# Optimization experiments

Hardware: AMD Instinct MI355X
Metric: run time of the kernel (lower is better)

## Reference

```python
import jax, jax.numpy as jnp
import numpy as np

HEADS = 8
DIM_HEAD = 64
QUERY_DIM = 512
INNER = HEADS * DIM_HEAD
DIAG_OFFSET = 1
T_TEMP = 1.0
NEG_INF = -1e9  # used via -inf below; kept for clarity


def setup_inputs() -> dict:
    key = jax.random.key(0)
    ks = jax.random.split(key, 8)
    b, s, f = 2, 2048, 16
    x = jax.random.normal(ks[0], (b, s, f, QUERY_DIM), dtype=jnp.float32)
    pos_bias = jax.random.normal(ks[1], (HEADS, f, f), dtype=jnp.float32)
    w_scale = 0.02
    Wq = jax.random.normal(ks[2], (QUERY_DIM, INNER), dtype=jnp.float32) * w_scale
    Wk = jax.random.normal(ks[3], (QUERY_DIM, INNER), dtype=jnp.float32) * w_scale
    Wv = jax.random.normal(ks[4], (QUERY_DIM, INNER), dtype=jnp.float32) * w_scale
    Wo = jax.random.normal(ks[5], (INNER, QUERY_DIM), dtype=jnp.float32) * w_scale
    bo = jax.random.normal(ks[6], (QUERY_DIM,), dtype=jnp.float32) * w_scale
    return {"x": x, "pos_bias": pos_bias, "Wq": Wq, "Wk": Wk, "Wv": Wv, "Wo": Wo, "bo": bo}


def reference(x, pos_bias, Wq, Wk, Wv, Wo, bo):
    # x: [b, s, f, c] -- temporal attention over the frame axis f per spatial token
    b, s, f, _ = x.shape
    scale = DIM_HEAD ** -0.5
    q = (x @ Wq).reshape(b, s, f, HEADS, DIM_HEAD)
    k = (x @ Wk).reshape(b, s, f, HEADS, DIM_HEAD)
    v = (x @ Wv).reshape(b, s, f, HEADS, DIM_HEAD)
    # scores over frames: [b, s, h, f_q, f_k]
    w = jnp.einsum('bsihd,bsjhd->bshij', q * scale, k)
    w = w + pos_bias[None, None]  # [h, f, f] relative position bias
    # attend_prev_only causal mask (strict, diag_offset=1)
    causal = jnp.triu(jnp.ones((f, f), dtype=jnp.float32), k=DIAG_OFFSET)
    w = w + jnp.where(causal == 1.0, -jnp.inf, 0.0)
    # faithful to source: subtract row max, then softmax with temperature
    w = w - jax.lax.stop_gradient(jnp.max(w, axis=-1, keepdims=True))
    p = jax.nn.softmax(w.astype(jnp.float32) / T_TEMP, axis=-1).astype(w.dtype)
    out = jnp.einsum('bshij,bsjhd->bsihd', p, v).reshape(b, s, f, INNER)
    return out @ Wo + bo
```

## Files before the change

### kernel.cpp

```cpp
#include <hip/hip_runtime.h>

typedef unsigned short u16;
typedef __attribute__((ext_vector_type(8))) unsigned short u16x8;
typedef __attribute__((ext_vector_type(8))) __bf16 bf16x8;
typedef __attribute__((ext_vector_type(4))) float f32x4;

#define M_ROWS 65536
#define KDIM   512
#define NKT    8

typedef __attribute__((address_space(1))) const void gconst_void;
typedef __attribute__((address_space(3))) void lds_void;

static __device__ __forceinline__ u16 f2bf(float f) {
  unsigned u = __builtin_bit_cast(unsigned, f);
  u += 0x7FFFu + ((u >> 16) & 1u);
  return (u16)(u >> 16);
}

static __device__ __forceinline__ f32x4 mfma_bf16(u16x8 a, u16x8 b, f32x4 c) {
  return __builtin_amdgcn_mfma_f32_16x16x32_bf16(
      __builtin_bit_cast(bf16x8, a), __builtin_bit_cast(bf16x8, b), c, 0, 0, 0);
}

__global__ void conv_x(const float* __restrict__ x, u16* __restrict__ xb) {
  const size_t t = (size_t)blockIdx.x * 256 + threadIdx.x;
  f32x4 a = *(const f32x4*)(x + t * 8);
  f32x4 b = *(const f32x4*)(x + t * 8 + 4);
  u16x8 w;
#pragma unroll
  for (int e = 0; e < 4; ++e) { w[e] = f2bf(a[e]); w[e + 4] = f2bf(b[e]); }
  *(u16x8*)(xb + t * 8) = w;
}

__global__ void convW_qkv_t(const float* __restrict__ Wq, const float* __restrict__ Wk,
                            const float* __restrict__ Wv, u16* __restrict__ Wt) {
  __shared__ float tile[32][33];
  const int bn = blockIdx.x * 32;
  const int bk = blockIdx.y * 32;
  const int tx = threadIdx.x & 31, ty = threadIdx.x >> 5;
  const float* W = (bn < 512) ? Wq : ((bn < 1024) ? Wk : Wv);
  const int coln = bn & 511;
#pragma unroll
  for (int r = 0; r < 32; r += 8)
    tile[ty + r][tx] = W[(size_t)(bk + ty + r) * 512 + coln + tx];
  __syncthreads();
#pragma unroll
  for (int r = 0; r < 32; r += 8)
    Wt[(size_t)(bn + ty + r) * 512 + bk + tx] = f2bf(tile[tx][ty + r]);
}

__global__ void convWo_t(const float* __restrict__ Wo, u16* __restrict__ Wt) {
  __shared__ float tile[32][33];
  const int bn = blockIdx.x * 32;
  const int bk = blockIdx.y * 32;
  const int tx = threadIdx.x & 31, ty = threadIdx.x >> 5;
#pragma unroll
  for (int r = 0; r < 32; r += 8)
    tile[ty + r][tx] = Wo[(size_t)(bk + ty + r) * 512 + bn + tx];
  __syncthreads();
#pragma unroll
  for (int r = 0; r < 32; r += 8)
    Wt[(size_t)(bn + ty + r) * 512 + bk + tx] = f2bf(tile[tx][ty + r]);
}

__global__ __launch_bounds__(512, 4)
void gemm_qkv_attn(const u16* __restrict__ A, const u16* __restrict__ Wt,
                   const float* __restrict__ pos_bias, u16* __restrict__ attnbuf) {
  __shared__ __attribute__((aligned(16))) u16 smem[40960];
  u16* Ab   = smem;
  u16* Bb   = smem + 16384;
  u16* qkvT = smem;
  u16* Pl   = smem + 25600;

  const int tid  = threadIdx.x;
  const int lane = tid & 63;
  const int wid  = tid >> 6;
  const int wm   = wid >> 2;
  const int wn   = wid & 3;
  const int lg   = lane >> 4;
  const int lc   = lane & 15;
  const int srow = lane >> 3;
  const int sg   = (lane & 7) ^ srow;

  const int nwg  = gridDim.x;
  const int cpx  = nwg >> 3;
  const int flat = blockIdx.x;
  const int swz  = (flat & 7) * cpx + (flat >> 3);
  const int mt   = swz >> 3;
  const int h    = swz & 7;
  const int row0 = mt * 128;

  auto stageA = [&](int buf, int unit, int kt) {
    const int rl = unit * 64 + wid * 8;
    const u16* src = A + (size_t)(row0 + rl + srow) * KDIM + kt * 64 + sg * 8;
    __builtin_amdgcn_global_load_lds((gconst_void*)src,
                                     (lds_void*)&Ab[buf * 8192 + rl * 64], 16, 0, 0);
  };
  auto stageB = [&](int buf, int unit, int kt) {
    const int rl = unit * 64 + wid * 8;
    const int grow = unit * 512 + h * 64 + wid * 8 + srow;
    const u16* src = Wt + (size_t)grow * KDIM + kt * 64 + sg * 8;
    __builtin_amdgcn_global_load_lds((gconst_void*)src,
                                     (lds_void*)&Bb[buf * 12288 + rl * 64], 16, 0, 0);
  };

  f32x4 acc[4][3];
#pragma unroll
  for (int mi = 0; mi < 4; ++mi)
#pragma unroll
    for (int ni = 0; ni < 3; ++ni) acc[mi][ni] = (f32x4){0.f, 0.f, 0.f, 0.f};

  stageA(0, 0, 0); stageA(0, 1, 0);
  stageB(0, 0, 0); stageB(0, 1, 0); stageB(0, 2, 0);
  asm volatile("s_waitcnt vmcnt(0)" ::: "memory");
  __builtin_amdgcn_s_barrier();

  for (int t = 0; t < NKT; ++t) {
    const int  c   = t & 1;
    const bool pre = (t + 1) < NKT;

    if (pre) {
      stageA(c ^ 1, 0, t + 1); stageA(c ^ 1, 1, t + 1);
      stageB(c ^ 1, 0, t + 1); stageB(c ^ 1, 1, t + 1); stageB(c ^ 1, 2, t + 1);
    }

#pragma unroll
    for (int ks = 0; ks < 2; ++ks) {
      const int gsw = ((ks * 4 + lg) ^ (lc & 7)) << 3;
      u16x8 bfr[3], af[4];
#pragma unroll
      for (int ni = 0; ni < 3; ++ni)
        bfr[ni] = *(const u16x8*)&Bb[c * 12288 + (wn * 48 + ni * 16 + lc) * 64 + gsw];
#pragma unroll
      for (int i = 0; i < 4; ++i)
        af[i] = *(const u16x8*)&Ab[c * 8192 + (wm * 64 + i * 16 + lc) * 64 + gsw];
#pragma unroll
      for (int i = 0; i < 4; ++i)
#pragma unroll
        for (int ni = 0; ni < 3; ++ni)
          acc[i][ni] = mfma_bf16(af[i], bfr[ni], acc[i][ni]);
    }

    asm volatile("s_waitcnt vmcnt(0)" ::: "memory");
    __builtin_amdgcn_s_barrier();
  }

#pragma unroll
  for (int mi = 0; mi < 4; ++mi)
#pragma unroll
    for (int ni = 0; ni < 3; ++ni) {
      const int col = wn * 48 + ni * 16 + lc;
      const int rb  = wm * 64 + mi * 16 + lg * 4;
#pragma unroll
      for (int r = 0; r < 4; ++r)
        qkvT[(rb + r) * 200 + col] = f2bf(acc[mi][ni][r]);
    }
  __syncthreads();

  const float scale = 0.125f;
  const f32x4 zf = {0.f, 0.f, 0.f, 0.f};
  const int rb = wid * 16;
  const int qb = (rb + lc) * 200;

  u16x8 aq0 = *(const u16x8*)&qkvT[qb + 0  + lg * 8];
  u16x8 aq1 = *(const u16x8*)&qkvT[qb + 32 + lg * 8];
  u16x8 bk0 = *(const u16x8*)&qkvT[qb + 64 + lg * 8];
  u16x8 bk1 = *(const u16x8*)&qkvT[qb + 96 + lg * 8];
  f32x4 s = mfma_bf16(aq0, bk0, zf);
  s = mfma_bf16(aq1, bk1, s);

  const int pb = wid * 256;
#pragma unroll
  for (int r = 0; r < 4; ++r) {
    const int i = lg * 4 + r;
    float sv = s[r] * scale + pos_bias[h * 256 + i * 16 + lc];
    if (lc > i) sv = -1e30f;
    float m = sv;
#pragma unroll
    for (int off = 8; off >= 1; off >>= 1) m = fmaxf(m, __shfl_xor(m, off));
    float e = __expf(sv - m);
    float sm = e;
#pragma unroll
    for (int off = 8; off >= 1; off >>= 1) sm += __shfl_xor(sm, off);
    Pl[pb + i * 16 + lc] = f2bf(e / sm);
  }
  asm volatile("s_waitcnt lgkmcnt(0)" ::: "memory");

  u16x8 ap = {0, 0, 0, 0, 0, 0, 0, 0};
  if (lane < 32) ap = *(const u16x8*)&Pl[pb + lc * 16 + lg * 8];

#pragma unroll
  for (int nd = 0; nd < 4; ++nd) {
    u16x8 bv = {0, 0, 0, 0, 0, 0, 0, 0};
    if (lane < 32) {
#pragma unroll
      for (int jj = 0; jj < 8; ++jj) {
        const int j = lg * 8 + jj;
        bv[jj] = qkvT[(rb + j) * 200 + 128 + nd * 16 + lc];
      }
    }
    f32x4 o = mfma_bf16(ap, bv, zf);
#pragma unroll
    for (int r = 0; r < 4; ++r) {
      const int i = lg * 4 + r;
      attnbuf[(size_t)(row0 + rb + i) * 512 + h * 64 + nd * 16 + lc] = f2bf(o[r]);
    }
  }
}

__global__ __launch_bounds__(512, 2)
void gemm_out(const u16* __restrict__ A, const u16* __restrict__ Bt,
              float* __restrict__ C, const float* __restrict__ bias) {
  __shared__ __attribute__((aligned(16))) u16 smem[65536];
  u16* Ab = smem;
  u16* Bb = smem + 49152;

  const int tid  = threadIdx.x;
  const int lane = tid & 63;
  const int wid  = tid >> 6;
  const int wm   = wid >> 1;
  const int wn   = wid & 1;
  const int lg   = lane >> 4;
  const int lc   = lane & 15;
  const int srow = lane >> 3;
  const int sg   = (lane & 7) ^ srow;

  const int nwg  = gridDim.x;
  const int cpx  = nwg >> 3;
  const int flat = blockIdx.x;
  const int swz  = (flat & 7) * cpx + (flat >> 3);
  const int mt   = swz >> 2;
  const int nt   = swz & 3;
  const int row0 = mt * 256, col0 = nt * 128;

  auto stageA = [&](int buf, int unit, int kt) {
    const int rl = unit * 64 + wid * 8;
    const u16* src = A + (size_t)(row0 + rl + srow) * KDIM + kt * 64 + sg * 8;
    __builtin_amdgcn_global_load_lds((gconst_void*)src,
                                     (lds_void*)&Ab[buf * 16384 + rl * 64], 16, 0, 0);
  };
  auto stageB = [&](int buf, int unit, int kt) {
    const int rl = unit * 64 + wid * 8;
    const u16* src = Bt + (size_t)(col0 + rl + srow) * KDIM + kt * 64 + sg * 8;
    __builtin_amdgcn_global_load_lds((gconst_void*)src,
                                     (lds_void*)&Bb[buf * 8192 + rl * 64], 16, 0, 0);
  };

  f32x4 acc[4][4];
#pragma unroll
  for (int mi = 0; mi < 4; ++mi)
#pragma unroll
    for (int ni = 0; ni < 4; ++ni) acc[mi][ni] = (f32x4){0.f, 0.f, 0.f, 0.f};

#pragma unroll
  for (int u = 0; u < 4; ++u) stageA(0, u, 0);
#pragma unroll
  for (int u = 0; u < 2; ++u) stageB(0, u, 0);
#pragma unroll
  for (int u = 0; u < 4; ++u) stageA(1, u, 1);

  for (int t = 0; t < NKT; ++t) {
    const int  ab   = t % 3;
    const int  bb   = t & 1;
    const bool preB = (t + 1) < NKT;
    const bool preA = (t + 2) < NKT;
    const int  ab2  = (t + 2) % 3;

    if (t < NKT - 1) asm volatile("s_waitcnt vmcnt(4)" ::: "memory");
    else             asm volatile("s_waitcnt vmcnt(0)" ::: "memory");
    __builtin_amdgcn_s_barrier();

    if (preB) { stageB(bb ^ 1, 0, t + 1); stageB(bb ^ 1, 1, t + 1); }
    if (preA) { stageA(ab2, 0, t + 2); stageA(ab2, 1, t + 2);
                stageA(ab2, 2, t + 2); stageA(ab2, 3, t + 2); }

#pragma unroll
    for (int ks = 0; ks < 2; ++ks) {
      const int gsw = ((ks * 4 + lg) ^ (lc & 7)) << 3;
      u16x8 bfr[4], af[4];
#pragma unroll
      for (int ni = 0; ni < 4; ++ni)
        bfr[ni] = *(const u16x8*)&Bb[bb * 8192 + (wn * 64 + ni * 16 + lc) * 64 + gsw];
#pragma unroll
      for (int i = 0; i < 4; ++i)
        af[i] = *(const u16x8*)&Ab[ab * 16384 + (wm * 64 + i * 16 + lc) * 64 + gsw];
#pragma unroll
      for (int i = 0; i < 4; ++i)
#pragma unroll
        for (int ni = 0; ni < 4; ++ni)
          acc[i][ni] = mfma_bf16(af[i], bfr[ni], acc[i][ni]);
    }
  }

  const int gmb = row0 + wm * 64;
  const int gnb = col0 + wn * 64;
#pragma unroll
  for (int mi = 0; mi < 4; ++mi)
#pragma unroll
    for (int ni = 0; ni < 4; ++ni) {
      const int gm = gmb + mi * 16 + lg * 4;
      const int gn = gnb + ni * 16 + lc;
      const float bv = bias[gn];
      f32x4 v = acc[mi][ni];
#pragma unroll
      for (int r = 0; r < 4; ++r) C[(size_t)(gm + r) * 512 + gn] = v[r] + bv;
    }
}

extern "C" void kernel_launch(void* const* d_in, const int* in_sizes, int n_in,
                              void* d_out, int out_size, void* d_ws, size_t ws_size,
                              hipStream_t stream) {
  const float* x        = (const float*)d_in[0];
  const float* pos_bias = (const float*)d_in[1];
  const float* Wq       = (const float*)d_in[2];
  const float* Wk       = (const float*)d_in[3];
  const float* Wv       = (const float*)d_in[4];
  const float* Wo       = (const float*)d_in[5];
  const float* bo       = (const float*)d_in[6];
  float* out            = (float*)d_out;

  u16* xb      = (u16*)d_ws;
  u16* attnbuf = xb + (size_t)M_ROWS * 512;
  u16* Wo_t    = attnbuf + (size_t)M_ROWS * 512;
  u16* Wqkv_t  = (u16*)d_out;

  conv_x<<<dim3(M_ROWS * KDIM / (256 * 8)), dim3(256), 0, stream>>>(x, xb);
  convW_qkv_t<<<dim3(48, 16), dim3(256), 0, stream>>>(Wq, Wk, Wv, Wqkv_t);
  gemm_qkv_attn<<<dim3(4096), dim3(512), 0, stream>>>(xb, Wqkv_t, pos_bias, attnbuf);
  convWo_t<<<dim3(16, 16), dim3(256), 0, stream>>>(Wo, Wo_t);
  gemm_out<<<dim3(1024), dim3(512), 0, stream>>>(attnbuf, Wo_t, out, bo);
}
```

Measured before the change: 210.7 us.

## Shrink output GEMM tile to 128x128 with double-buffered LDS and higher occupancy

The output projection GEMM moves from a 256x128 tile with a triple-buffered A and double-buffered B pipeline to a 128x128 tile with a simple double buffer. The grid doubles to 2048 workgroups, LDS per block drops from 128KB to 64KB, and launch bounds ask for 4 blocks per CU. The goal is more waves per CU to hide latency, and a grid that spreads more evenly over the CUs. In exchange, each block reuses the B tile across fewer rows, so global traffic per FLOP goes up. Each iteration also now ends with a full vmcnt(0) wait and barrier, which reduces how much loads overlap with compute.

```diff
diff --git a/kernel.cpp b/kernel.cpp
--- a/kernel.cpp
+++ b/kernel.cpp
@@ -209,18 +209,18 @@
   }
 }
 
-__global__ __launch_bounds__(512, 2)
+__global__ __launch_bounds__(512, 4)
 void gemm_out(const u16* __restrict__ A, const u16* __restrict__ Bt,
               float* __restrict__ C, const float* __restrict__ bias) {
-  __shared__ __attribute__((aligned(16))) u16 smem[65536];
+  __shared__ __attribute__((aligned(16))) u16 smem[32768];
   u16* Ab = smem;
-  u16* Bb = smem + 49152;
+  u16* Bb = smem + 16384;
 
   const int tid  = threadIdx.x;
   const int lane = tid & 63;
   const int wid  = tid >> 6;
-  const int wm   = wid >> 1;
-  const int wn   = wid & 1;
+  const int wm   = wid >> 2;
+  const int wn   = wid & 3;
   const int lg   = lane >> 4;
   const int lc   = lane & 15;
   const int srow = lane >> 3;
@@ -232,13 +232,13 @@
   const int swz  = (flat & 7) * cpx + (flat >> 3);
   const int mt   = swz >> 2;
   const int nt   = swz & 3;
-  const int row0 = mt * 256, col0 = nt * 128;
+  const int row0 = mt * 128, col0 = nt * 128;
 
   auto stageA = [&](int buf, int unit, int kt) {
     const int rl = unit * 64 + wid * 8;
     const u16* src = A + (size_t)(row0 + rl + srow) * KDIM + kt * 64 + sg * 8;
     __builtin_amdgcn_global_load_lds((gconst_void*)src,
-                                     (lds_void*)&Ab[buf * 16384 + rl * 64], 16, 0, 0);
+                                     (lds_void*)&Ab[buf * 8192 + rl * 64], 16, 0, 0);
   };
   auto stageB = [&](int buf, int unit, int kt) {
     const int rl = unit * 64 + wid * 8;
@@ -247,58 +247,53 @@
                                      (lds_void*)&Bb[buf * 8192 + rl * 64], 16, 0, 0);
   };
 
-  f32x4 acc[4][4];
+  f32x4 acc[4][2];
 #pragma unroll
   for (int mi = 0; mi < 4; ++mi)
 #pragma unroll
-    for (int ni = 0; ni < 4; ++ni) acc[mi][ni] = (f32x4){0.f, 0.f, 0.f, 0.f};
-
-#pragma unroll
-  for (int u = 0; u < 4; ++u) stageA(0, u, 0);
-#pragma unroll
-  for (int u = 0; u < 2; ++u) stageB(0, u, 0);
-#pragma unroll
-  for (int u = 0; u < 4; ++u) stageA(1, u, 1);
+    for (int ni = 0; ni < 2; ++ni) acc[mi][ni] = (f32x4){0.f, 0.f, 0.f, 0.f};
+
+  stageA(0, 0, 0); stageA(0, 1, 0);
+  stageB(0, 0, 0); stageB(0, 1, 0);
+  asm volatile("s_waitcnt vmcnt(0)" ::: "memory");
+  __builtin_amdgcn_s_barrier();
 
   for (int t = 0; t < NKT; ++t) {
-    const int  ab   = t % 3;
-    const int  bb   = t & 1;
-    const bool preB = (t + 1) < NKT;
-    const bool preA = (t + 2) < NKT;
-    const int  ab2  = (t + 2) % 3;
-
-    if (t < NKT - 1) asm volatile("s_waitcnt vmcnt(4)" ::: "memory");
-    else             asm volatile("s_waitcnt vmcnt(0)" ::: "memory");
-    __builtin_amdgcn_s_barrier();
-
-    if (preB) { stageB(bb ^ 1, 0, t + 1); stageB(bb ^ 1, 1, t + 1); }
-    if (preA) { stageA(ab2, 0, t + 2); stageA(ab2, 1, t + 2);
-                stageA(ab2, 2, t + 2); stageA(ab2, 3, t + 2); }
+    const int  c   = t & 1;
+    const bool pre = (t + 1) < NKT;
+
+    if (pre) {
+      stageA(c ^ 1, 0, t + 1); stageA(c ^ 1, 1, t + 1);
+      stageB(c ^ 1, 0, t + 1); stageB(c ^ 1, 1, t + 1);
+    }
 
 #pragma unroll
     for (int ks = 0; ks < 2; ++ks) {
       const int gsw = ((ks * 4 + lg) ^ (lc & 7)) << 3;
-      u16x8 bfr[4], af[4];
-#pragma unroll
-      for (int ni = 0; ni < 4; ++ni)
-        bfr[ni] = *(const u16x8*)&Bb[bb * 8192 + (wn * 64 + ni * 16 + lc) * 64 + gsw];
+      u16x8 bfr[2], af[4];
+#pragma unroll
+      for (int ni = 0; ni < 2; ++ni)
+        bfr[ni] = *(const u16x8*)&Bb[c * 8192 + (wn * 32 + ni * 16 + lc) * 64 + gsw];
 #pragma unroll
       for (int i = 0; i < 4; ++i)
-        af[i] = *(const u16x8*)&Ab[ab * 16384 + (wm * 64 + i * 16 + lc) * 64 + gsw];
+        af[i] = *(const u16x8*)&Ab[c * 8192 + (wm * 64 + i * 16 + lc) * 64 + gsw];
 #pragma unroll
       for (int i = 0; i < 4; ++i)
 #pragma unroll
-        for (int ni = 0; ni < 4; ++ni)
+        for (int ni = 0; ni < 2; ++ni)
           acc[i][ni] = mfma_bf16(af[i], bfr[ni], acc[i][ni]);
     }
+
+    asm volatile("s_waitcnt vmcnt(0)" ::: "memory");
+    __builtin_amdgcn_s_barrier();
   }
 
   const int gmb = row0 + wm * 64;
-  const int gnb = col0 + wn * 64;
+  const int gnb = col0 + wn * 32;
 #pragma unroll
   for (int mi = 0; mi < 4; ++mi)
 #pragma unroll
-    for (int ni = 0; ni < 4; ++ni) {
+    for (int ni = 0; ni < 2; ++ni) {
       const int gm = gmb + mi * 16 + lg * 4;
       const int gn = gnb + ni * 16 + lc;
       const float bv = bias[gn];
@@ -329,5 +324,5 @@
   convW_qkv_t<<<dim3(48, 16), dim3(256), 0, stream>>>(Wq, Wk, Wv, Wqkv_t);
   gemm_qkv_attn<<<dim3(4096), dim3(512), 0, stream>>>(xb, Wqkv_t, pos_bias, attnbuf);
   convWo_t<<<dim3(16, 16), dim3(256), 0, stream>>>(Wo, Wo_t);
-  gemm_out<<<dim3(1024), dim3(512), 0, stream>>>(attnbuf, Wo_t, out, bo);
-}
+  gemm_out<<<dim3(2048), dim3(512), 0, stream>>>(attnbuf, Wo_t, out, bo);
+}
```

Result: no change. 210.5 us, median of 2 (-0.1%).
